# Kernel tuning notes

Measured on AMD Instinct MI355X. Metric: run time of the kernel, lower is better.

## Reference

```python
import jax, jax.numpy as jnp
import numpy as np

B, M, D, H, C = 256, 512, 768, 8, 768


def setup_inputs() -> dict:
    key = jax.random.key(0)
    ks = jax.random.split(key, 12)
    rn = lambda k, shp, s=1.0: jax.random.normal(k, shp, dtype=jnp.float32) * s
    w = 1.0 / np.sqrt(D)
    return dict(
        controller_state=rn(ks[0], (B, C)),
        write_data=rn(ks[1], (B, D)),
        memory=rn(ks[2], (M, D), 0.1),
        in_proj_w=rn(ks[3], (3 * D, D), w), in_proj_b=jnp.zeros((3 * D,), jnp.float32),
        out_w=rn(ks[4], (D, D), w), out_b=jnp.zeros((D,), jnp.float32),
        read_w=rn(ks[5], (D, C), w), read_b=jnp.zeros((D,), jnp.float32),
        write_w=rn(ks[6], (D, C), w), write_b=jnp.zeros((D,), jnp.float32),
        erase_w=rn(ks[7], (D, C), w), erase_b=jnp.zeros((D,), jnp.float32),
        ug_w=rn(ks[8], (1, C + D), w), ug_b=jnp.zeros((1,), jnp.float32),
        fg_w=rn(ks[9], (1, C + D), w), fg_b=jnp.zeros((1,), jnp.float32),
    )


def _mha(q, kv, in_proj_w, in_proj_b, out_w, out_b, num_heads):
    # q: [B,1,D] query, kv: [B,M,D] keys=values. Matches torch.nn.MultiheadAttention
    # (batch_first, eval mode -> no dropout, average_attn_weights=True).
    b, m, d = kv.shape
    dh = d // num_heads
    wq, wk, wv = jnp.split(in_proj_w, 3, axis=0)
    bq, bk, bv = jnp.split(in_proj_b, 3, axis=0)
    qh = (q @ wq.T + bq).reshape(b, 1, num_heads, dh).transpose(0, 2, 1, 3)   # [B,H,1,dh]
    kh = (kv @ wk.T + bk).reshape(b, m, num_heads, dh).transpose(0, 2, 1, 3)  # [B,H,M,dh]
    vh = (kv @ wv.T + bv).reshape(b, m, num_heads, dh).transpose(0, 2, 1, 3)
    scores = jnp.einsum('bhqd,bhkd->bhqk', qh, kh) / jnp.sqrt(jnp.float32(dh))
    attn = jax.nn.softmax(scores, axis=-1)                                    # [B,H,1,M]
    ctx = jnp.einsum('bhqk,bhkd->bhqd', attn, vh)
    ctx = ctx.transpose(0, 2, 1, 3).reshape(b, 1, d)
    out = ctx @ out_w.T + out_b
    return out, attn.mean(axis=1)  # out [B,1,D], weights averaged over heads [B,1,M]


def reference(controller_state, write_data, memory, in_proj_w, in_proj_b,
              out_w, out_b, read_w, read_b, write_w, write_b,
              erase_w, erase_b, ug_w, ug_b, fg_w, fg_b):
    b = controller_state.shape[0]
    memory_batch = jnp.broadcast_to(memory[None], (b,) + memory.shape)        # [B,M,D]

    read_key = (controller_state @ read_w.T + read_b)[:, None, :]             # [B,1,D]
    read_data, _ = _mha(read_key, memory_batch, in_proj_w, in_proj_b, out_w, out_b, H)
    read_data = read_data[:, 0, :]                                            # [B,D]

    write_key = (controller_state @ write_w.T + write_b)[:, None, :]
    erase_vec = jax.nn.sigmoid(controller_state @ erase_w.T + erase_b)[:, None, :]  # [B,1,D]
    _, write_weights = _mha(write_key, memory_batch, in_proj_w, in_proj_b, out_w, out_b, H)
    ww = write_weights[:, 0, :]                                               # [B,M]

    combined = jnp.concatenate([controller_state, read_data], axis=-1)        # [B,C+D]
    ug = jax.nn.sigmoid(combined @ ug_w.T + ug_b)                             # [B,1]
    fg = jax.nn.sigmoid(combined @ fg_w.T + fg_b)                             # [B,1]

    erase_term = ww[:, :, None] * erase_vec * fg[:, :, None]                  # [B,M,D]
    write_term = ww[:, :, None] * write_data[:, None, :] * ug[:, :, None]     # [B,M,D]
    updated_memory = memory_batch + (write_term - erase_term)
    return read_data, updated_memory
```

## Files before the change

kernel.cpp:

```cpp
#include <hip/hip_runtime.h>
#include <hip/hip_bf16.h>
#include <math.h>

#define B_ 256
#define M_ 512
#define D_ 768
#define H_ 8
#define DH_ 96
#define C_ 768

typedef float  f32x4_t __attribute__((ext_vector_type(4)));
typedef short  s16x8   __attribute__((ext_vector_type(8)));
typedef unsigned short u16;

__device__ __forceinline__ u16 cvt_bf16(float f) {
    __hip_bfloat16 h = __float2bfloat16(f);
    union { __hip_bfloat16 h; u16 u; } v; v.h = h;
    return v.u;
}
__device__ __forceinline__ float bf16_f32(u16 h) {
    union { unsigned int u; float f; } v; v.u = ((unsigned int)h) << 16;
    return v.f;
}

#define ACC_INIT {{0,0,0,0},{0,0,0,0},{0,0,0,0},{0,0,0,0}}
#define SCALE_ 0.10206207261596577f

template<int BK>
__device__ __forceinline__ void mm64b(
    const u16* __restrict__ A, int lda, const u16* __restrict__ B, int ldb,
    int ksteps, int bRowClamp, u16* lA, u16* lB, f32x4_t* acc, int nfrag)
{
    constexpr int NL = BK / 32;
    const int t = threadIdx.x;
    const int srow = t >> 2, kq = t & 3;
    const int l = t & 63, w = t >> 6;
    const int brow = srow < bRowClamp ? srow : bRowClamp;

    s16x8 va[NL], vb[NL];
    #pragma unroll
    for (int c = 0; c < NL; ++c) {
        const int ko = (kq * NL + c) * 8;
        va[c] = *reinterpret_cast<const s16x8*>(A + (size_t)srow * lda + ko);
        vb[c] = *reinterpret_cast<const s16x8*>(B + (size_t)brow * ldb + ko);
    }

    for (int ks = 0; ks < ksteps; ++ks) {
        __syncthreads();
        #pragma unroll
        for (int c = 0; c < NL; ++c) {
            const int kb = kq * NL + c;
            *reinterpret_cast<s16x8*>(lA + (kb * 64 + srow) * 8) = va[c];
            *reinterpret_cast<s16x8*>(lB + (kb * 64 + srow) * 8) = vb[c];
        }
        __syncthreads();
        if (ks + 1 < ksteps) {
            #pragma unroll
            for (int c = 0; c < NL; ++c) {
                const int ko = (ks + 1) * BK + (kq * NL + c) * 8;
                va[c] = *reinterpret_cast<const s16x8*>(A + (size_t)srow * lda + ko);
                vb[c] = *reinterpret_cast<const s16x8*>(B + (size_t)brow * ldb + ko);
            }
        }
        #pragma unroll
        for (int ksub = 0; ksub < NL; ++ksub) {
            const int kb = (l >> 4) + ksub * 4;
            s16x8 af = *reinterpret_cast<const s16x8*>(lA + (kb * 64 + w * 16 + (l & 15)) * 8);
            #pragma unroll
            for (int nb = 0; nb < 4; ++nb) {
                if (nb < nfrag) {
                    s16x8 bf = *reinterpret_cast<const s16x8*>(lB + (kb * 64 + nb * 16 + (l & 15)) * 8);
                    acc[nb] = __builtin_amdgcn_mfma_f32_16x16x32_bf16(af, bf, acc[nb], 0, 0, 0);
                }
            }
        }
    }
}

__device__ __forceinline__ void epilogue_f32(
    const f32x4_t* acc, float* out, int ldo, int m0, int n0,
    const float* bias, int act, int nfrag)
{
    const int t = threadIdx.x, l = t & 63, w = t >> 6;
    const int mbase = m0 + w * 16 + (l >> 4) * 4;
    #pragma unroll
    for (int nb = 0; nb < 4; ++nb) {
        if (nb >= nfrag) break;
        const int col = n0 + nb * 16 + (l & 15);
        const float bv = bias ? bias[col] : 0.0f;
        #pragma unroll
        for (int r = 0; r < 4; ++r) {
            float v = acc[nb][r] + bv;
            if (act) v = 1.0f / (1.0f + expf(-v));
            out[(size_t)(mbase + r) * ldo + col] = v;
        }
    }
}

__device__ __forceinline__ void epilogue_bf16(
    const f32x4_t* acc, u16* out, int ldo, int m0, int n0,
    const float* bias, int nfrag)
{
    const int t = threadIdx.x, l = t & 63, w = t >> 6;
    const int mbase = m0 + w * 16 + (l >> 4) * 4;
    #pragma unroll
    for (int nb = 0; nb < 4; ++nb) {
        if (nb >= nfrag) break;
        const int col = n0 + nb * 16 + (l & 15);
        const float bv = bias ? bias[col] : 0.0f;
        #pragma unroll
        for (int r = 0; r < 4; ++r)
            out[(size_t)(mbase + r) * ldo + col] = cvt_bf16(acc[nb][r] + bv);
    }
}

__global__ __launch_bounds__(256) void conv_kernel(
    const float* __restrict__ mem, const float* __restrict__ cs,
    const float* __restrict__ ipw, const float* __restrict__ rw,
    const float* __restrict__ www, const float* __restrict__ ew,
    const float* __restrict__ outw, const float* __restrict__ outb,
    const float* __restrict__ ugw, const float* __restrict__ ugb,
    const float* __restrict__ fgw, const float* __restrict__ fgb,
    u16* __restrict__ memb, u16* __restrict__ csb, u16* __restrict__ ipwb,
    u16* __restrict__ rwb, u16* __restrict__ wwwb, u16* __restrict__ ewb,
    u16* __restrict__ outwb, float* __restrict__ vg, float* __restrict__ gc)
{
    __shared__ float sred[256];
    const int bid = blockIdx.x, t = threadIdx.x;

    if (bid < 2304) {
        const float* src; u16* dst; int base;
        if      (bid < 192)  { src = mem;  dst = memb;  base = bid; }
        else if (bid < 288)  { src = cs;   dst = csb;   base = bid - 192; }
        else if (bid < 1152) { src = ipw;  dst = ipwb;  base = bid - 288; }
        else if (bid < 1440) { src = rw;   dst = rwb;   base = bid - 1152; }
        else if (bid < 1728) { src = www;  dst = wwwb;  base = bid - 1440; }
        else if (bid < 2016) { src = ew;   dst = ewb;   base = bid - 1728; }
        else                 { src = outw; dst = outwb; base = bid - 2016; }
        const size_t i = ((size_t)base * 256 + t) * 8;
        float4 x = *reinterpret_cast<const float4*>(src + i);
        float4 y = *reinterpret_cast<const float4*>(src + i + 4);
        s16x8 o;
        o[0]=cvt_bf16(x.x); o[1]=cvt_bf16(x.y); o[2]=cvt_bf16(x.z); o[3]=cvt_bf16(x.w);
        o[4]=cvt_bf16(y.x); o[5]=cvt_bf16(y.y); o[6]=cvt_bf16(y.z); o[7]=cvt_bf16(y.w);
        *reinterpret_cast<s16x8*>(dst + i) = o;
    } else {
        const int lid = bid - 2304;
        const int v = lid / 12, kt = lid % 12;
        const float* gw = v == 0 ? ugw : fgw;
        const int c = t & 63, g = t >> 6;
        const int col = kt * 64 + c;
        float acc = 0.f;
        #pragma unroll 4
        for (int i = 0; i < 192; ++i) {
            const int row = g * 192 + i;
            acc += outw[(size_t)row * 768 + col] * gw[768 + row];
        }
        sred[t] = acc;
        __syncthreads();
        if (g == 0)
            vg[v * 768 + col] = sred[c] + sred[64 + c] + sred[128 + c] + sred[192 + c];
        if (kt == 0) {
            __syncthreads();
            float cp = outb[t] * gw[768 + t] + outb[t + 256] * gw[768 + t + 256]
                     + outb[t + 512] * gw[768 + t + 512];
            sred[t] = cp; __syncthreads();
            #pragma unroll
            for (int off = 128; off > 0; off >>= 1) {
                if (t < off) sred[t] += sred[t + off];
                __syncthreads();
            }
            if (t == 0) gc[v] = sred[0] + (v == 0 ? ugb[0] : fgb[0]);
        }
    }
}

__global__ __launch_bounds__(256) void stage1_kernel(
    const u16* __restrict__ memb, const u16* __restrict__ csb,
    const u16* __restrict__ ipwb, const float* __restrict__ ipb,
    const u16* __restrict__ rwb, const float* __restrict__ rb,
    const u16* __restrict__ wwwb, const float* __restrict__ ww_b,
    const u16* __restrict__ ewb, const float* __restrict__ eb,
    u16* __restrict__ khb, u16* __restrict__ vhT,
    u16* __restrict__ rwkeysb, float* __restrict__ erase)
{
    __shared__ u16 lA[8192], lB[8192];
    f32x4_t acc[4] = ACC_INIT;
    const int bid = blockIdx.x;
    if (bid < 192) {
        const int mt = bid / 24, nt = bid % 24;
        mm64b<64>(memb + (size_t)mt * 64 * 768, 768,
                  ipwb + (size_t)768 * 768 + (size_t)nt * 64 * 768, 768,
                  12, 63, lA, lB, acc, 4);
        const int t = threadIdx.x, l = t & 63, w = t >> 6;
        const int mbase = mt * 64 + w * 16 + (l >> 4) * 4;
        if (nt < 12) {
            #pragma unroll
            for (int nb = 0; nb < 4; ++nb) {
                const int col = nt * 64 + nb * 16 + (l & 15);
                const float bv = ipb[768 + col];
                #pragma unroll
                for (int r = 0; r < 4; ++r)
                    khb[(size_t)(mbase + r) * 768 + col] = cvt_bf16(acc[nb][r] + bv);
            }
        } else {
            #pragma unroll
            for (int nb = 0; nb < 4; ++nb) {
                const int cg = (nt - 12) * 64 + nb * 16 + (l & 15);
                const int h = cg / 96, d = cg % 96;
                const float bv = ipb[1536 + cg];
                u16* dst = vhT + ((size_t)h * 96 + d) * 512;
                #pragma unroll
                for (int r = 0; r < 4; ++r)
                    dst[mbase + r] = cvt_bf16(acc[nb][r] + bv);
            }
        }
    } else if (bid < 240) {
        const int lid = bid - 192, mt = lid / 12, nt = lid % 12;
        mm64b<64>(csb + (size_t)mt * 64 * 768, 768, rwb + (size_t)nt * 64 * 768, 768,
                  12, 63, lA, lB, acc, 4);
        epilogue_bf16(acc, rwkeysb, 768, mt * 64, nt * 64, rb, 4);
    } else if (bid < 288) {
        const int lid = bid - 240, mt = lid / 12, nt = lid % 12;
        mm64b<64>(csb + (size_t)mt * 64 * 768, 768, wwwb + (size_t)nt * 64 * 768, 768,
                  12, 63, lA, lB, acc, 4);
        epilogue_bf16(acc, rwkeysb + (size_t)256 * 768, 768, mt * 64, nt * 64, ww_b, 4);
    } else {
        const int lid = bid - 288, mt = lid / 12, nt = lid % 12;
        mm64b<64>(csb + (size_t)mt * 64 * 768, 768, ewb + (size_t)nt * 64 * 768, 768,
                  12, 63, lA, lB, acc, 4);
        epilogue_f32(acc, erase, 768, mt * 64, nt * 64, eb, 1, 4);
    }
}

__global__ __launch_bounds__(256) void stage2_kernel(
    const u16* __restrict__ rwkeysb, const u16* __restrict__ ipwb,
    const float* __restrict__ ipb, u16* __restrict__ qrwb,
    const u16* __restrict__ vhT, const float* __restrict__ vg,
    float* __restrict__ zv)
{
    const int bid = blockIdx.x, t = threadIdx.x;
    if (bid < 96) {
        __shared__ u16 lA[8192], lB[8192];
        f32x4_t acc[4] = ACC_INIT;
        const int mt = bid / 12, nt = bid % 12;
        mm64b<64>(rwkeysb + (size_t)mt * 64 * 768, 768, ipwb + (size_t)nt * 64 * 768, 768,
                  12, 63, lA, lB, acc, 4);
        epilogue_bf16(acc, qrwb, 768, mt * 64, nt * 64, ipb, 4);
    } else {
        const int lid = bid - 96;
        const int v = lid >> 3, h = lid & 7;
        float a0 = 0.f, a1 = 0.f;
        for (int d = 0; d < 96; ++d) {
            const float g = vg[v * 768 + h * 96 + d];
            const u16* row = vhT + ((size_t)h * 96 + d) * 512;
            a0 += bf16_f32(row[t]) * g;
            a1 += bf16_f32(row[t + 256]) * g;
        }
        zv[(size_t)v * 4096 + h * 512 + t]       = a0;
        zv[(size_t)v * 4096 + h * 512 + t + 256] = a1;
    }
}

__global__ __launch_bounds__(256) void scores_kernel(
    const u16* __restrict__ qrwb, const u16* __restrict__ khb, u16* __restrict__ E)
{
    __shared__ u16 lA[2048], lB[2048];
    f32x4_t acc[4] = ACC_INIT;
    const int h = blockIdx.y;
    const int mt = blockIdx.x >> 3, nt = blockIdx.x & 7;
    mm64b<32>(qrwb + (size_t)mt * 64 * 768 + h * 96, 768,
              khb + (size_t)nt * 64 * 768 + h * 96, 768, 3, 63, lA, lB, acc, 4);
    const int t = threadIdx.x, l = t & 63, w = t >> 6;
    const int mbase = mt * 64 + w * 16 + (l >> 4) * 4;
    #pragma unroll
    for (int nb = 0; nb < 4; ++nb) {
        const int col = nt * 64 + nb * 16 + (l & 15);
        #pragma unroll
        for (int r = 0; r < 4; ++r) {
            const float e = expf(fminf(acc[nb][r] * SCALE_, 30.0f));
            E[((size_t)h * 512 + mbase + r) * 512 + col] = cvt_bf16(e);
        }
    }
}

__global__ __launch_bounds__(256) void pvww_kernel(
    const u16* __restrict__ E, const u16* __restrict__ vhT, u16* __restrict__ ctxb,
    float* __restrict__ wwb,
    const float* __restrict__ cs, const float* __restrict__ ugw,
    const float* __restrict__ fgw, const float* __restrict__ zv,
    const float* __restrict__ gc, float* __restrict__ ugfg)
{
    const int bid = blockIdx.x, t = threadIdx.x;
    if (bid < 64) {
        __shared__ u16 lA[8192], lB[8192];
        __shared__ float rinv[64];
        f32x4_t acc[4] = ACC_INIT;
        const int h = bid >> 3;
        const int mt = (bid >> 1) & 3, nt = bid & 1;
        const int n0 = nt * 64;
        const int nfrag = nt == 0 ? 4 : 2;
        const int bclamp = nt == 0 ? 63 : 31;

        const u16* A  = E + ((size_t)h * 512 + mt * 64) * 512;
        const u16* Bv = vhT + ((size_t)h * 96 + n0) * 512;

        const int srow = t >> 2, kq = t & 3;
        const int l = t & 63, w = t >> 6;
        const int brow = srow < bclamp ? srow : bclamp;

        s16x8 va[2], vb[2];
        #pragma unroll
        for (int c = 0; c < 2; ++c) {
            const int ko = (kq * 2 + c) * 8;
            va[c] = *reinterpret_cast<const s16x8*>(A + (size_t)srow * 512 + ko);
            vb[c] = *reinterpret_cast<const s16x8*>(Bv + (size_t)brow * 512 + ko);
        }

        float rs = 0.f;
        for (int ks = 0; ks < 8; ++ks) {
            __syncthreads();
            #pragma unroll
            for (int c = 0; c < 2; ++c) {
                const int kb = kq * 2 + c;
                *reinterpret_cast<s16x8*>(lA + (kb * 64 + srow) * 8) = va[c];
                *reinterpret_cast<s16x8*>(lB + (kb * 64 + srow) * 8) = vb[c];
            }
            #pragma unroll
            for (int c = 0; c < 2; ++c)
                #pragma unroll
                for (int j = 0; j < 8; ++j)
                    rs += bf16_f32((u16)va[c][j]);
            __syncthreads();
            if (ks + 1 < 8) {
                #pragma unroll
                for (int c = 0; c < 2; ++c) {
                    const int ko = (ks + 1) * 64 + (kq * 2 + c) * 8;
                    va[c] = *reinterpret_cast<const s16x8*>(A + (size_t)srow * 512 + ko);
                    vb[c] = *reinterpret_cast<const s16x8*>(Bv + (size_t)brow * 512 + ko);
                }
            }
            #pragma unroll
            for (int ksub = 0; ksub < 2; ++ksub) {
                const int kb = (l >> 4) + ksub * 4;
                s16x8 af = *reinterpret_cast<const s16x8*>(lA + (kb * 64 + w * 16 + (l & 15)) * 8);
                #pragma unroll
                for (int nb = 0; nb < 4; ++nb) {
                    if (nb < nfrag) {
                        s16x8 bf = *reinterpret_cast<const s16x8*>(lB + (kb * 64 + nb * 16 + (l & 15)) * 8);
                        acc[nb] = __builtin_amdgcn_mfma_f32_16x16x32_bf16(af, bf, acc[nb], 0, 0, 0);
                    }
                }
            }
        }
        rs += __shfl_xor(rs, 1);
        rs += __shfl_xor(rs, 2);
        if (kq == 0) rinv[srow] = 1.0f / rs;
        __syncthreads();

        const int mbase = w * 16 + (l >> 4) * 4;
        #pragma unroll
        for (int nb = 0; nb < 4; ++nb) {
            if (nb >= nfrag) break;
            const int col = n0 + nb * 16 + (l & 15);
            #pragma unroll
            for (int r = 0; r < 4; ++r) {
                const float v = acc[nb][r] * rinv[mbase + r];
                ctxb[(size_t)(mt * 64 + mbase + r) * 768 + h * 96 + col] = cvt_bf16(v);
            }
        }
    } else if (bid < 320) {
        const int b = bid - 64;
        __shared__ float linv8[8];
        const int w = t >> 6, l = t & 63;
        #pragma unroll
        for (int hh = 0; hh < 2; ++hh) {
            const int h = w * 2 + hh;
            const u16* row = E + ((size_t)h * 512 + 256 + b) * 512;
            float s = 0.f;
            #pragma unroll
            for (int c = 0; c < 8; ++c) s += bf16_f32(row[c * 64 + l]);
            #pragma unroll
            for (int off = 32; off > 0; off >>= 1) s += __shfl_xor(s, off);
            if (l == 0) linv8[h] = 1.0f / s;
        }
        __syncthreads();
        #pragma unroll
        for (int mm_ = 0; mm_ < 2; ++mm_) {
            const int m = t + mm_ * 256;
            float s = 0.f;
            #pragma unroll
            for (int h = 0; h < H_; ++h)
                s += bf16_f32(E[((size_t)h * 512 + 256 + b) * 512 + m]) * linv8[h];
            wwb[(size_t)b * 512 + m] = s * 0.125f;
        }
    } else {
        const int b = bid - 320;
        __shared__ float wred[4][3];
        __shared__ float gacc[2];
        __shared__ float red[8];
        const int w = t >> 6, l = t & 63;
        if (t == 0) { gacc[0] = 0.f; gacc[1] = 0.f; }

        float pu = 0.f, pf = 0.f;
        #pragma unroll
        for (int c = 0; c < 3; ++c) {
            const int i = t + c * 256;
            const float cv = cs[(size_t)b * 768 + i];
            pu += cv * ugw[i];
            pf += cv * fgw[i];
        }

        for (int h = 0; h < 8; ++h) {
            float s0 = 0.f, su = 0.f, sf = 0.f;
            #pragma unroll
            for (int mm_ = 0; mm_ < 2; ++mm_) {
                const int m = t + mm_ * 256;
                const float e = bf16_f32(E[((size_t)h * 512 + b) * 512 + m]);
                s0 += e;
                su += e * zv[(size_t)h * 512 + m];
                sf += e * zv[4096 + (size_t)h * 512 + m];
            }
            #pragma unroll
            for (int off = 32; off > 0; off >>= 1) {
                s0 += __shfl_xor(s0, off);
                su += __shfl_xor(su, off);
                sf += __shfl_xor(sf, off);
            }
            if (l == 0) { wred[w][0] = s0; wred[w][1] = su; wred[w][2] = sf; }
            __syncthreads();
            if (t == 0) {
                const float S0 = wred[0][0] + wred[1][0] + wred[2][0] + wred[3][0];
                const float Su = wred[0][1] + wred[1][1] + wred[2][1] + wred[3][1];
                const float Sf = wred[0][2] + wred[1][2] + wred[2][2] + wred[3][2];
                gacc[0] += Su / S0;
                gacc[1] += Sf / S0;
            }
            __syncthreads();
        }

        #pragma unroll
        for (int off = 32; off > 0; off >>= 1) {
            pu += __shfl_xor(pu, off);
            pf += __shfl_xor(pf, off);
        }
        if (l == 0) { red[w] = pu; red[4 + w] = pf; }
        __syncthreads();
        if (t == 0) {
            const float tu = red[0] + red[1] + red[2] + red[3] + gacc[0] + gc[0];
            const float tf = red[4] + red[5] + red[6] + red[7] + gacc[1] + gc[1];
            ugfg[2 * b]     = 1.0f / (1.0f + expf(-tu));
            ugfg[2 * b + 1] = 1.0f / (1.0f + expf(-tf));
        }
    }
}

__global__ __launch_bounds__(256) void final_kernel(
    const u16* __restrict__ ctxb, const u16* __restrict__ outwb,
    const float* __restrict__ outb, float* __restrict__ rd_out,
    const float* __restrict__ mem, const float* __restrict__ wwb,
    const float* __restrict__ wdta, const float* __restrict__ erase,
    const float* __restrict__ ugfg, float* __restrict__ mem_out)
{
    __shared__ u16 lA[8192], lB[8192];
    const int bid = blockIdx.x, t = threadIdx.x;
    if (bid < 48) {
        f32x4_t acc[4] = ACC_INIT;
        const int mt = bid / 12, nt = bid % 12;
        mm64b<64>(ctxb + (size_t)mt * 64 * 768, 768, outwb + (size_t)nt * 64 * 768, 768,
                  12, 63, lA, lB, acc, 4);
        epilogue_f32(acc, rd_out, 768, mt * 64, nt * 64, outb, 0, 4);
    } else {
        const int u = bid - 48;
        const int b  = u >> 6;
        const int m0 = (u & 63) << 3;
        const float ug = ugfg[2 * b], fg = ugfg[2 * b + 1];
        const f32x4_t* m4 = reinterpret_cast<const f32x4_t*>(mem);
        f32x4_t* o4 = reinterpret_cast<f32x4_t*>(mem_out + (size_t)b * 393216);
        const float* wrow = wdta  + (size_t)b * 768;
        const float* erow = erase + (size_t)b * 768;
        #pragma unroll
        for (int ph = 0; ph < 6; ++ph) {
            const int c = t + ph * 256;
            const int m = m0 + c / 192;
            const int d4 = c % 192;
            const float w = wwb[(size_t)b * 512 + m];
            const f32x4_t wd = *reinterpret_cast<const f32x4_t*>(wrow + d4 * 4);
            const f32x4_t er = *reinterpret_cast<const f32x4_t*>(erow + d4 * 4);
            const f32x4_t dd = wd * ug - er * fg;
            f32x4_t mm = m4[(size_t)m * 192 + d4];
            f32x4_t r = mm + w * dd;
            __builtin_nontemporal_store(r, &o4[(size_t)m * 192 + d4]);
        }
    }
}

extern "C" void kernel_launch(void* const* d_in, const int* in_sizes, int n_in,
                              void* d_out, int out_size, void* d_ws, size_t ws_size,
                              hipStream_t stream)
{
    const float* cs   = (const float*)d_in[0];
    const float* wdta = (const float*)d_in[1];
    const float* mem  = (const float*)d_in[2];
    const float* ipw  = (const float*)d_in[3];
    const float* ipb  = (const float*)d_in[4];
    const float* outw = (const float*)d_in[5];
    const float* outb = (const float*)d_in[6];
    const float* rw   = (const float*)d_in[7];
    const float* rb   = (const float*)d_in[8];
    const float* ww_w = (const float*)d_in[9];
    const float* ww_b = (const float*)d_in[10];
    const float* ew   = (const float*)d_in[11];
    const float* eb   = (const float*)d_in[12];
    const float* ugw  = (const float*)d_in[13];
    const float* ugb  = (const float*)d_in[14];
    const float* fgw  = (const float*)d_in[15];
    const float* fgb  = (const float*)d_in[16];

    float* rd_out  = (float*)d_out;
    float* mem_out = (float*)d_out + B_ * D_;

    float* S0 = mem_out;
    u16*   memb    = (u16*)(S0 + 0);
    u16*   csb     = (u16*)(S0 + 196608);
    u16*   ipwb    = (u16*)(S0 + 294912);
    u16*   rwb     = (u16*)(S0 + 1179648);
    u16*   wwwb    = (u16*)(S0 + 1474560);
    u16*   ewb     = (u16*)(S0 + 1769472);
    u16*   khb     = (u16*)(S0 + 2064384);
    u16*   vhT     = (u16*)(S0 + 2260992);
    u16*   rwkeysb = (u16*)(S0 + 2457600);
    u16*   qrwb    = (u16*)(S0 + 2654208);

    float* ws    = (float*)d_ws;
    float* erase = ws;
    u16*   ctxb  = (u16*)(ws + 196608);
    u16*   E     = (u16*)(ws + 294912);
    float* vg    =        ws + 1343488;
    float* gc    =        ws + 1345024;
    float* ugfg  =        ws + 1345040;
    float* wwb   =        ws + 1345552;
    u16*   outwb = (u16*)(ws + 1476624);
    float* zv    =        ws + 1771536;

    conv_kernel<<<2328, 256, 0, stream>>>(mem, cs, ipw, rw, ww_w, ew, outw, outb,
                                          ugw, ugb, fgw, fgb,
                                          memb, csb, ipwb, rwb, wwwb, ewb, outwb,
                                          vg, gc);
    stage1_kernel<<<336, 256, 0, stream>>>(memb, csb, ipwb, ipb, rwb, rb, wwwb, ww_b,
                                           ewb, eb, khb, vhT, rwkeysb, erase);
    stage2_kernel<<<112, 256, 0, stream>>>(rwkeysb, ipwb, ipb, qrwb, vhT, vg, zv);
    scores_kernel<<<dim3(64, 8), 256, 0, stream>>>(qrwb, khb, E);
    pvww_kernel<<<576, 256, 0, stream>>>(E, vhT, ctxb, wwb,
                                         cs, ugw, fgw, zv, gc, ugfg);
    final_kernel<<<16432, 256, 0, stream>>>(ctxb, outwb, outb, rd_out,
                                            mem, wwb, wdta, erase, ugfg, mem_out);
}
```

Baseline: 125.3 us.

## Fuse Q projection into scores kernel, keeping per-head Q tile in LDS

```diff
diff --git a/kernel.cpp b/kernel.cpp
--- a/kernel.cpp
+++ b/kernel.cpp
@@ -233,22 +233,122 @@
     }
 }
 
-__global__ __launch_bounds__(256) void stage2_kernel(
+__global__ __launch_bounds__(256) void qscores_kernel(
     const u16* __restrict__ rwkeysb, const u16* __restrict__ ipwb,
-    const float* __restrict__ ipb, u16* __restrict__ qrwb,
+    const float* __restrict__ ipb, const u16* __restrict__ khb,
+    u16* __restrict__ E,
     const u16* __restrict__ vhT, const float* __restrict__ vg,
     float* __restrict__ zv)
 {
     const int bid = blockIdx.x, t = threadIdx.x;
-    if (bid < 96) {
-        __shared__ u16 lA[8192], lB[8192];
-        f32x4_t acc[4] = ACC_INIT;
-        const int mt = bid / 12, nt = bid % 12;
-        mm64b<64>(rwkeysb + (size_t)mt * 64 * 768, 768, ipwb + (size_t)nt * 64 * 768, 768,
-                  12, 63, lA, lB, acc, 4);
-        epilogue_bf16(acc, qrwb, 768, mt * 64, nt * 64, ipb, 4);
+    if (bid < 64) {
+        __shared__ u16 lA[4096];
+        __shared__ u16 lB[8192];
+        __shared__ u16 lQ[6144];
+        __shared__ u16 lS[6144];
+        const int mt = bid >> 3, h = bid & 7;
+        const int l = t & 63, w = t >> 6;
+
+        f32x4_t acc[6] = {{0,0,0,0},{0,0,0,0},{0,0,0,0},{0,0,0,0},{0,0,0,0},{0,0,0,0}};
+        const u16* A  = rwkeysb + (size_t)mt * 64 * 768;
+        const u16* Bq = ipwb + (size_t)h * 96 * 768;
+        const int arow = t >> 2, akq = t & 3;
+        const int brow = t >> 1, bkq = t & 1;
+        const int browc = brow < 95 ? brow : 95;
+
+        s16x8 va[2], vb[4];
+        #pragma unroll
+        for (int c = 0; c < 2; ++c)
+            va[c] = *reinterpret_cast<const s16x8*>(A + (size_t)arow * 768 + (akq * 2 + c) * 8);
+        #pragma unroll
+        for (int c = 0; c < 4; ++c)
+            vb[c] = *reinterpret_cast<const s16x8*>(Bq + (size_t)browc * 768 + (bkq * 4 + c) * 8);
+
+        for (int ks = 0; ks < 12; ++ks) {
+            __syncthreads();
+            #pragma unroll
+            for (int c = 0; c < 2; ++c)
+                *reinterpret_cast<s16x8*>(lA + ((akq * 2 + c) * 64 + arow) * 8) = va[c];
+            #pragma unroll
+            for (int c = 0; c < 4; ++c)
+                *reinterpret_cast<s16x8*>(lB + ((bkq * 4 + c) * 128 + brow) * 8) = vb[c];
+            __syncthreads();
+            if (ks + 1 < 12) {
+                #pragma unroll
+                for (int c = 0; c < 2; ++c)
+                    va[c] = *reinterpret_cast<const s16x8*>(A + (size_t)arow * 768 + (ks + 1) * 64 + (akq * 2 + c) * 8);
+                #pragma unroll
+                for (int c = 0; c < 4; ++c)
+                    vb[c] = *reinterpret_cast<const s16x8*>(Bq + (size_t)browc * 768 + (ks + 1) * 64 + (bkq * 4 + c) * 8);
+            }
+            #pragma unroll
+            for (int ksub = 0; ksub < 2; ++ksub) {
+                const int kb = (l >> 4) + ksub * 4;
+                s16x8 af = *reinterpret_cast<const s16x8*>(lA + (kb * 64 + w * 16 + (l & 15)) * 8);
+                #pragma unroll
+                for (int nb = 0; nb < 6; ++nb) {
+                    s16x8 bf = *reinterpret_cast<const s16x8*>(lB + (kb * 128 + nb * 16 + (l & 15)) * 8);
+                    acc[nb] = __builtin_amdgcn_mfma_f32_16x16x32_bf16(af, bf, acc[nb], 0, 0, 0);
+                }
+            }
+        }
+
+        __syncthreads();
+        {
+            const int qrow0 = w * 16 + (l >> 4) * 4;
+            #pragma unroll
+            for (int nb = 0; nb < 6; ++nb) {
+                const int d = nb * 16 + (l & 15);
+                const float bv = ipb[h * 96 + d];
+                #pragma unroll
+                for (int r = 0; r < 4; ++r)
+                    lQ[((d >> 3) * 64 + qrow0 + r) * 8 + (d & 7)] = cvt_bf16(acc[nb][r] + bv);
+            }
+        }
+        __syncthreads();
+
+        const int srow = t >> 2, kq = t & 3;
+        s16x8 vs[3];
+        #pragma unroll
+        for (int c = 0; c < 3; ++c)
+            vs[c] = *reinterpret_cast<const s16x8*>(khb + (size_t)srow * 768 + h * 96 + (kq * 3 + c) * 8);
+
+        for (int nt = 0; nt < 8; ++nt) {
+            __syncthreads();
+            #pragma unroll
+            for (int c = 0; c < 3; ++c)
+                *reinterpret_cast<s16x8*>(lS + ((kq * 3 + c) * 64 + srow) * 8) = vs[c];
+            __syncthreads();
+            if (nt + 1 < 8) {
+                #pragma unroll
+                for (int c = 0; c < 3; ++c)
+                    vs[c] = *reinterpret_cast<const s16x8*>(
+                        khb + (size_t)((nt + 1) * 64 + srow) * 768 + h * 96 + (kq * 3 + c) * 8);
+            }
+            f32x4_t sacc[4] = ACC_INIT;
+            #pragma unroll
+            for (int ks2 = 0; ks2 < 3; ++ks2) {
+                const int kb = ks2 * 4 + (l >> 4);
+                s16x8 af = *reinterpret_cast<const s16x8*>(lQ + (kb * 64 + w * 16 + (l & 15)) * 8);
+                #pragma unroll
+                for (int nb = 0; nb < 4; ++nb) {
+                    s16x8 bf = *reinterpret_cast<const s16x8*>(lS + (kb * 64 + nb * 16 + (l & 15)) * 8);
+                    sacc[nb] = __builtin_amdgcn_mfma_f32_16x16x32_bf16(af, bf, sacc[nb], 0, 0, 0);
+                }
+            }
+            const int mbase = mt * 64 + w * 16 + (l >> 4) * 4;
+            #pragma unroll
+            for (int nb = 0; nb < 4; ++nb) {
+                const int col = nt * 64 + nb * 16 + (l & 15);
+                #pragma unroll
+                for (int r = 0; r < 4; ++r) {
+                    const float e = expf(fminf(sacc[nb][r] * SCALE_, 30.0f));
+                    E[((size_t)h * 512 + mbase + r) * 512 + col] = cvt_bf16(e);
+                }
+            }
+        }
     } else {
-        const int lid = bid - 96;
+        const int lid = bid - 64;
         const int v = lid >> 3, h = lid & 7;
         float a0 = 0.f, a1 = 0.f;
         for (int d = 0; d < 96; ++d) {
@@ -259,28 +359,6 @@
         }
         zv[(size_t)v * 4096 + h * 512 + t]       = a0;
         zv[(size_t)v * 4096 + h * 512 + t + 256] = a1;
-    }
-}
-
-__global__ __launch_bounds__(256) void scores_kernel(
-    const u16* __restrict__ qrwb, const u16* __restrict__ khb, u16* __restrict__ E)
-{
-    __shared__ u16 lA[2048], lB[2048];
-    f32x4_t acc[4] = ACC_INIT;
-    const int h = blockIdx.y;
-    const int mt = blockIdx.x >> 3, nt = blockIdx.x & 7;
-    mm64b<32>(qrwb + (size_t)mt * 64 * 768 + h * 96, 768,
-              khb + (size_t)nt * 64 * 768 + h * 96, 768, 3, 63, lA, lB, acc, 4);
-    const int t = threadIdx.x, l = t & 63, w = t >> 6;
-    const int mbase = mt * 64 + w * 16 + (l >> 4) * 4;
-    #pragma unroll
-    for (int nb = 0; nb < 4; ++nb) {
-        const int col = nt * 64 + nb * 16 + (l & 15);
-        #pragma unroll
-        for (int r = 0; r < 4; ++r) {
-            const float e = expf(fminf(acc[nb][r] * SCALE_, 30.0f));
-            E[((size_t)h * 512 + mbase + r) * 512 + col] = cvt_bf16(e);
-        }
     }
 }
 
@@ -530,7 +608,6 @@
     u16*   khb     = (u16*)(S0 + 2064384);
     u16*   vhT     = (u16*)(S0 + 2260992);
     u16*   rwkeysb = (u16*)(S0 + 2457600);
-    u16*   qrwb    = (u16*)(S0 + 2654208);
 
     float* ws    = (float*)d_ws;
     float* erase = ws;
@@ -549,8 +626,7 @@
                                           vg, gc);
     stage1_kernel<<<336, 256, 0, stream>>>(memb, csb, ipwb, ipb, rwb, rb, wwwb, ww_b,
                                            ewb, eb, khb, vhT, rwkeysb, erase);
-    stage2_kernel<<<112, 256, 0, stream>>>(rwkeysb, ipwb, ipb, qrwb, vhT, vg, zv);
-    scores_kernel<<<dim3(64, 8), 256, 0, stream>>>(qrwb, khb, E);
+    qscores_kernel<<<80, 256, 0, stream>>>(rwkeysb, ipwb, ipb, khb, E, vhT, vg, zv);
     pvww_kernel<<<576, 256, 0, stream>>>(E, vhT, ctxb, wwb,
                                          cs, ugw, fgw, zv, gc, ugfg);
     final_kernel<<<16432, 256, 0, stream>>>(ctxb, outwb, outb, rd_out,
```

After: 130.1 us. +3.8%, slower.
